# Performance work log

Hardware: AMD Instinct MI355X
Metric: run time of the kernel (lower is better)

Reference implementation:

```python
import jax, jax.numpy as jnp
import numpy as np

D_MODEL = 1024
D_STATE = 32
K = 4
B_SZ = 2
L_SEQ = 1024
DT_MIN = 0.001
DT_MAX = 0.2


def setup_inputs() -> dict:
    key = jax.random.key(0)
    ks = jax.random.split(key, 10)
    n = lambda k, s: jax.random.normal(k, s, dtype=jnp.float32)
    D, N = D_MODEL, D_STATE
    return {
        "x": n(ks[0], (B_SZ, L_SEQ, D)),
        "W_in": 0.02 * n(ks[1], (D, 2 * D)),
        "b_in": jnp.zeros((2 * D,), jnp.float32),
        "conv_w": 0.2 * n(ks[2], (D, 1, K)),   # depthwise conv kernel (O,I/g,K)
        "conv_b": jnp.zeros((D,), jnp.float32),
        "A_log": -2.0 + 0.1 * n(ks[3], (D, N)),
        "wB": 0.02 * n(ks[4], (D, N)),
        "bB": jnp.zeros((D, N), jnp.float32),
        "wC": 0.02 * n(ks[5], (D, N)),
        "bC": jnp.zeros((D, N), jnp.float32),
        "W_dt": 0.02 * n(ks[6], (D, D)),
        "b_dt": jnp.zeros((D,), jnp.float32),
        "W_out": 0.02 * n(ks[7], (D, D)),
        "b_out": jnp.zeros((D,), jnp.float32),
        "ln_g": jnp.ones((D,), jnp.float32),
        "ln_b": jnp.zeros((D,), jnp.float32),
    }


def reference(x, W_in, b_in, conv_w, conv_b, A_log, wB, bB, wC, bC,
              W_dt, b_dt, W_out, b_out, ln_g, ln_b):
    Bsz, L, D = x.shape
    N = A_log.shape[1]
    residual = x
    # input projection -> x path and gate z
    xz = x @ W_in + b_in
    xp, z = jnp.split(xz, 2, axis=-1)
    # causal depthwise conv1d (left-pad k-1)
    xt = jnp.swapaxes(xp, 1, 2)  # (B, D, L)
    y = jax.lax.conv_general_dilated(
        xt, conv_w, window_strides=(1,), padding=[(K - 1, 0)],
        dimension_numbers=("NCH", "OIH", "NCH"), feature_group_count=D)
    x_conv = jnp.swapaxes(y + conv_b[None, :, None], 1, 2)  # (B, L, D)
    xs = jax.nn.silu(x_conv)
    # selective SSM parameters
    A = -jnp.exp(jnp.clip(A_log, -5.0, 2.0))          # (D, N)
    Bt = xs[..., None] * wB + bB                      # (B, L, D, N) grouped 1x1 conv
    Ct = xs[..., None] * wC + bC                      # (B, L, D, N)
    dt = jnp.clip(jax.nn.softplus(xs @ W_dt + b_dt), DT_MIN, DT_MAX)  # (B, L, D)

    def step(states, inp):
        dt_i, B_i, C_i, x_i = inp  # (B,D), (B,D,N), (B,D,N), (B,D)
        A_bar = jnp.exp(jnp.clip(dt_i[..., None] * A, -10.0, 0.0))
        st = jnp.clip(states * A_bar + dt_i[..., None] * B_i * x_i[..., None],
                      -10.0, 10.0)
        return st, jnp.sum(C_i * st, axis=-1)

    states0 = jnp.zeros((Bsz, D, N), x.dtype)
    tl = lambda a: jnp.moveaxis(a, 1, 0)  # time-leading for scan
    _, ys = jax.lax.scan(step, states0, (tl(dt), tl(Bt), tl(Ct), tl(xs)))
    scan_out = jnp.moveaxis(ys, 0, 1) * jax.nn.silu(z)  # (B, L, D)
    out = scan_out @ W_out + b_out
    h = out + residual
    mu = jnp.mean(h, axis=-1, keepdims=True)
    var = jnp.var(h, axis=-1, keepdims=True)
    return (h - mu) / jnp.sqrt(var + 1e-5) * ln_g + ln_b
```

## Files before the change

### kernel.cpp

```cpp
#include <hip/hip_runtime.h>
#include <hip/hip_bf16.h>
#include <math.h>

#define D_MODEL 1024
#define D_STATE 32
#define LSEQ    1024
#define BSZ     2
#define MROWS   (BSZ*LSEQ)
#define NSEG    32
#define SEGL    (LSEQ/NSEG)
#define SCD     8
#define LOG2E   1.4426950408889634f

typedef unsigned short u16;
typedef unsigned int   u32;
typedef __bf16 bf16x8 __attribute__((ext_vector_type(8)));
typedef float  f32x4  __attribute__((ext_vector_type(4)));

__device__ __forceinline__ u16 f2b(float v) {
    unsigned int b = __float_as_uint(v);
    return (u16)((b + 0x7FFFu + ((b >> 16) & 1u)) >> 16);
}
__device__ __forceinline__ float b2f(u16 v) {
    return __uint_as_float((unsigned)v << 16);
}
__device__ __forceinline__ float softplus_clip(float v) {
    float sp = fmaxf(v, 0.f) + log1pf(__expf(-fabsf(v)));
    return fminf(fmaxf(sp, 0.001f), 0.2f);
}
__device__ __forceinline__ float silu(float v) {
    return v / (1.f + __expf(-v));
}

#define GLOAD16(g, l) __builtin_amdgcn_global_load_lds(                     \
    (__attribute__((address_space(1))) void*)(g),                           \
    (__attribute__((address_space(3))) void*)(l), 16, 0, 0)

__global__ __launch_bounds__(256)
void wprep_k(const float* __restrict__ W_in, const float* __restrict__ W_dt,
             const float* __restrict__ W_out, const float* __restrict__ x,
             u16* __restrict__ WinT, u16* __restrict__ WdtT,
             u16* __restrict__ WoutT, u16* __restrict__ xb) {
    int job = blockIdx.x;
    if (job >= 4096) {
        int i = (job - 4096) * 256 + threadIdx.x;
        float4 v = ((const float4*)x)[i];
        ushort4 o;
        o.x = f2b(v.x); o.y = f2b(v.y); o.z = f2b(v.z); o.w = f2b(v.w);
        ((ushort4*)xb)[i] = o;
        return;
    }
    const float* W; u16* Wt; int N;
    if (job < 2048)      { W = W_in;  Wt = WinT;  N = 2048; }
    else if (job < 3072) { W = W_dt;  Wt = WdtT;  N = 1024; job -= 2048; }
    else                 { W = W_out; Wt = WoutT; N = 1024; job -= 3072; }
    const int K = 1024;
    const int ntx = N >> 5;
    const int n0 = (job % ntx) << 5, k0 = (job / ntx) << 5;
    __shared__ u16 tile[32][33];
    const int tx = threadIdx.x & 31, ty = threadIdx.x >> 5;
#pragma unroll
    for (int r = 0; r < 32; r += 8)
        tile[r + ty][tx] = f2b(W[(size_t)(k0 + r + ty) * N + n0 + tx]);
    __syncthreads();
#pragma unroll
    for (int r = 0; r < 32; r += 8)
        Wt[(size_t)(n0 + r + ty) * K + k0 + tx] = tile[tx][r + ty];
}

template<int EPI, int OD>
__global__ __launch_bounds__(256)
void mgemm2_k(const u16* __restrict__ A, const u16* __restrict__ Bt,
              const float* __restrict__ bias, const float* __restrict__ res,
              void* __restrict__ Cv, int M, int N, int K) {
    __shared__ u16 As[2][4096];
    __shared__ u16 Bs[2][4096];
    const int t  = threadIdx.x;
    const int l  = t & 63;
    const int w  = t >> 6;
    const int wr = w >> 1, wc = w & 1;
    const int fr = l & 15, fq = l >> 4;

    const int nx  = N >> 6;
    const int nwg = (M >> 6) * nx;
    int wg = blockIdx.y * nx + blockIdx.x;
    int sw = (wg & 7) * (nwg >> 3) + (wg >> 3);
    const int bm = (sw / nx) << 6;
    const int bn = (sw % nx) << 6;

    const int srow = t >> 3;
    const int scol = ((t & 7) * 8) ^ ((srow & 7) << 3);
    const u16* Ap0 = A  + (size_t)(bm + srow)      * K + scol;
    const u16* Ap1 = A  + (size_t)(bm + 32 + srow) * K + scol;
    const u16* Bp0 = Bt + (size_t)(bn + srow)      * K + scol;
    const u16* Bp1 = Bt + (size_t)(bn + 32 + srow) * K + scol;

    f32x4 acc[2][2] = {};

#define STAGE2(buf, k0)                                      \
    GLOAD16(Ap0 + (k0), &As[buf][t * 8]);                    \
    GLOAD16(Ap1 + (k0), &As[buf][2048 + t * 8]);             \
    GLOAD16(Bp0 + (k0), &Bs[buf][t * 8]);                    \
    GLOAD16(Bp1 + (k0), &Bs[buf][2048 + t * 8]);

    STAGE2(0, 0)
    asm volatile("s_waitcnt vmcnt(0)" ::: "memory");
    __syncthreads();

    const int NT = K >> 6;
    int cur = 0;
    for (int ks = 0; ks < NT; ++ks) {
        if (ks + 1 < NT) { STAGE2(cur ^ 1, (ks + 1) << 6) }
        bf16x8 af[2][2], bf[2][2];
#pragma unroll
        for (int m = 0; m < 2; ++m) {
            const int r = wr * 32 + m * 16 + fr;
            const int xo = (r & 7) << 3;
#pragma unroll
            for (int kk = 0; kk < 2; ++kk)
                af[m][kk] = *(const bf16x8*)&As[cur][r * 64 + ((kk * 32 + fq * 8) ^ xo)];
        }
#pragma unroll
        for (int n = 0; n < 2; ++n) {
            const int c = wc * 32 + n * 16 + fr;
            const int xo = (c & 7) << 3;
#pragma unroll
            for (int kk = 0; kk < 2; ++kk)
                bf[n][kk] = *(const bf16x8*)&Bs[cur][c * 64 + ((kk * 32 + fq * 8) ^ xo)];
        }
#pragma unroll
        for (int m = 0; m < 2; ++m)
#pragma unroll
            for (int n = 0; n < 2; ++n)
#pragma unroll
                for (int kk = 0; kk < 2; ++kk)
                    acc[m][n] = __builtin_amdgcn_mfma_f32_16x16x32_bf16(
                        af[m][kk], bf[n][kk], acc[m][n], 0, 0, 0);
        asm volatile("s_waitcnt vmcnt(0)" ::: "memory");
        __syncthreads();
        cur ^= 1;
    }
#undef STAGE2

#pragma unroll
    for (int m = 0; m < 2; ++m) {
        const int row = bm + wr * 32 + m * 16 + fq * 4;
#pragma unroll
        for (int n = 0; n < 2; ++n) {
            const int col = bn + wc * 32 + n * 16 + fr;
            float bi = (EPI == 3) ? 0.f : bias[col];
#pragma unroll
            for (int j = 0; j < 4; ++j) {
                float v = acc[m][n][j];
                if (EPI == 3) v = softplus_clip(v + bias[row + j]);
                else          v += bi;
                if (EPI == 2) v += res[(size_t)(row + j) * N + col];
                if (OD == 1) ((u16*)Cv)[(size_t)(row + j) * N + col] = f2b(v);
                else         ((float*)Cv)[(size_t)(row + j) * N + col] = v;
            }
        }
    }
}

__global__ __launch_bounds__(256)
void convT_k(const u16* __restrict__ xz, const float* __restrict__ cw,
             const float* __restrict__ cb,
             u16* __restrict__ xsb, u16* __restrict__ xsT,
             u16* __restrict__ zsT) {
    const int l0 = blockIdx.x * 64;
    const int d0 = blockIdx.y * 64;
    const int b  = blockIdx.z;
    const int t  = threadIdx.x;
    __shared__ float xin[67][68];
    __shared__ float xo[64][69];
    const int lr = t >> 4, c4 = (t & 15) << 2;
    const u16* srcx = xz + ((size_t)b * LSEQ + l0 - 3) * 2048 + d0;
#pragma unroll
    for (int p = 0; p < 5; ++p) {
        int r = p * 16 + lr;
        if (r < 67) {
            float4 v = make_float4(0.f, 0.f, 0.f, 0.f);
            if (l0 + r >= 3) {
                ushort4 u = *(const ushort4*)(srcx + (size_t)r * 2048 + c4);
                v = make_float4(b2f(u.x), b2f(u.y), b2f(u.z), b2f(u.w));
            }
            *(float4*)&xin[r][c4] = v;
        }
    }
    __syncthreads();
    const int dd = t & 63;
    const int wv = t >> 6;
    float4 w4 = *(const float4*)(cw + ((size_t)(d0 + dd)) * 4);
    float cbv = cb[d0 + dd];
    float win[19];
#pragma unroll
    for (int i = 0; i < 19; ++i) win[i] = xin[wv * 16 + i][dd];
    u16* xrow = xsb + ((size_t)b * LSEQ + l0 + wv * 16) * D_MODEL + d0 + dd;
#pragma unroll
    for (int i = 0; i < 16; ++i) {
        float a = cbv;
        a = fmaf(win[i],     w4.x, a);
        a = fmaf(win[i + 1], w4.y, a);
        a = fmaf(win[i + 2], w4.z, a);
        a = fmaf(win[i + 3], w4.w, a);
        float r = silu(a);
        xrow[(size_t)i * D_MODEL] = f2b(r);
        xo[dd][wv * 16 + i] = r;
    }
    __syncthreads();
    {
        const int dr = t >> 2, ls = (t & 3) << 4;
        u16* dst = xsT + ((size_t)(d0 + dr)) * MROWS + (size_t)b * LSEQ + l0 + ls;
        ushort4 o[4];
#pragma unroll
        for (int j = 0; j < 16; ++j)
            ((u16*)o)[j] = f2b(xo[dr][ls + j]);
#pragma unroll
        for (int j = 0; j < 4; ++j)
            ((ushort4*)dst)[j] = o[j];
    }
    __syncthreads();
    const u16* srcz = xz + ((size_t)b * LSEQ + l0) * 2048 + 1024 + d0;
#pragma unroll
    for (int p = 0; p < 4; ++p) {
        int r = p * 16 + lr;
        ushort4 u = *(const ushort4*)(srcz + (size_t)r * 2048 + c4);
        xo[c4 + 0][r] = silu(b2f(u.x));
        xo[c4 + 1][r] = silu(b2f(u.y));
        xo[c4 + 2][r] = silu(b2f(u.z));
        xo[c4 + 3][r] = silu(b2f(u.w));
    }
    __syncthreads();
    {
        const int dr = t >> 2, ls = (t & 3) << 4;
        u16* dst = zsT + ((size_t)(d0 + dr)) * MROWS + (size_t)b * LSEQ + l0 + ls;
        ushort4 o[4];
#pragma unroll
        for (int j = 0; j < 16; ++j)
            ((u16*)o)[j] = f2b(xo[dr][ls + j]);
#pragma unroll
        for (int j = 0; j < 4; ++j)
            ((ushort4*)dst)[j] = o[j];
    }
}

__global__ __launch_bounds__(256, 4)
void scan_a(const u16* __restrict__ xsT, const u16* __restrict__ dtT,
            const float* __restrict__ A_log, const float* __restrict__ wB,
            const float* __restrict__ bB,
            float* __restrict__ Qbuf, float* __restrict__ sdtb) {
    const int t   = threadIdx.x;
    const int grp = t >> 5, g = t & 31;
    const int d   = blockIdx.x * SCD + grp;
    const int seg = blockIdx.y, b = blockIdx.z;
    const size_t chb = (size_t)d * MROWS + (size_t)b * LSEQ + (size_t)seg * SEGL;
    const int pi  = d * D_STATE + g;

    const float A2  = -__expf(fminf(fmaxf(A_log[pi], -5.f), 2.f)) * LOG2E;
    const float wB0 = wB[pi], bB0 = bB[pi];
    float s = 0.f;

    u16 xu = xsT[chb + g];
    u16 du = dtT[chb + g];
    float sdt = b2f(du);
    u32 pk = ((u32)xu << 16) | du;
#pragma unroll
    for (int h = 0; h < 2; ++h) {
        float av[16], dbv[16];
#pragma unroll
        for (int u = 0; u < 16; ++u) {
            u32 p = (u32)__shfl((int)pk, h * 16 + u, 32);
            float xa = __uint_as_float(p & 0xffff0000u);
            float da = __uint_as_float(p << 16);
            av[u]  = __builtin_amdgcn_exp2f(da * A2);
            dbv[u] = (da * xa) * fmaf(xa, wB0, bB0);
        }
#pragma unroll
        for (int u = 0; u < 16; ++u)
            s = fmaf(s, av[u], dbv[u]);
    }
    sdt += __shfl_xor(sdt, 1);
    sdt += __shfl_xor(sdt, 2);
    sdt += __shfl_xor(sdt, 4);
    sdt += __shfl_xor(sdt, 8);
    sdt += __shfl_xor(sdt, 16);
    const size_t qb = ((size_t)b * D_MODEL + d) * NSEG + seg;
    Qbuf[qb * 32 + g] = s;
    if (g == 0) sdtb[qb] = sdt;
}

__global__ __launch_bounds__(256, 4)
void scan_c(const u16* __restrict__ xsT, const u16* __restrict__ dtT,
            const u16* __restrict__ zsT,
            const float* __restrict__ A_log, const float* __restrict__ wB,
            const float* __restrict__ bB, const float* __restrict__ wC,
            const float* __restrict__ bC,
            const float* __restrict__ Qbuf, const float* __restrict__ sdtb,
            u16* __restrict__ so) {
    const int t   = threadIdx.x;
    const int grp = t >> 5, g = t & 31;
    const int d   = blockIdx.x * SCD + grp;
    const int seg = blockIdx.y, b = blockIdx.z;
    const size_t chb = (size_t)d * MROWS + (size_t)b * LSEQ + (size_t)seg * SEGL;
    const int pi  = d * D_STATE + g;

    const float A2  = -__expf(fminf(fmaxf(A_log[pi], -5.f), 2.f)) * LOG2E;
    const float wB0 = wB[pi], bB0 = bB[pi];
    const float wC0 = wC[pi], bC0 = bC[pi];

    float s = 0.f;
    const size_t qb = ((size_t)b * D_MODEL + d) * NSEG;
    for (int j = 0; j < seg; ++j) {
        float qj = Qbuf[(qb + j) * 32 + g];
        float pj = __builtin_amdgcn_exp2f(A2 * sdtb[qb + j]);
        s = fmaf(s, pj, qj);
    }

    __shared__ u16 tile[32][10];
    const size_t obase = ((size_t)b * LSEQ + (size_t)seg * SEGL) * D_MODEL
                       + blockIdx.x * SCD;

    {
        u16 xu = xsT[chb + g];
        u16 du = dtT[chb + g];
        float zw = b2f(zsT[chb + g]);
        u32 pk = ((u32)xu << 16) | du;
        float w_[32];
#pragma unroll
        for (int h = 0; h < 2; ++h) {
            float av[16], dbv[16], cv[16];
#pragma unroll
            for (int u = 0; u < 16; ++u) {
                u32 p = (u32)__shfl((int)pk, h * 16 + u, 32);
                float xa = __uint_as_float(p & 0xffff0000u);
                float da = __uint_as_float(p << 16);
                av[u]  = __builtin_amdgcn_exp2f(da * A2);
                dbv[u] = (da * xa) * fmaf(xa, wB0, bB0);
                cv[u]  = fmaf(xa, wC0, bC0);
            }
#pragma unroll
            for (int u = 0; u < 16; ++u) {
                s = fmaf(s, av[u], dbv[u]);
                w_[h * 16 + u] = cv[u] * s;
            }
        }
#pragma unroll
        for (int u = 0; u < 16; ++u) {
            float snd = (g & 16) ? w_[u] : w_[u + 16];
            float rcv = __shfl_xor(snd, 16);
            w_[u] = ((g & 16) ? w_[u + 16] : w_[u]) + rcv;
        }
#pragma unroll
        for (int u = 0; u < 8; ++u) {
            float snd = (g & 8) ? w_[u] : w_[u + 8];
            float rcv = __shfl_xor(snd, 8);
            w_[u] = ((g & 8) ? w_[u + 8] : w_[u]) + rcv;
        }
#pragma unroll
        for (int u = 0; u < 4; ++u) {
            float snd = (g & 4) ? w_[u] : w_[u + 4];
            float rcv = __shfl_xor(snd, 4);
            w_[u] = ((g & 4) ? w_[u + 4] : w_[u]) + rcv;
        }
#pragma unroll
        for (int u = 0; u < 2; ++u) {
            float snd = (g & 2) ? w_[u] : w_[u + 2];
            float rcv = __shfl_xor(snd, 2);
            w_[u] = ((g & 2) ? w_[u + 2] : w_[u]) + rcv;
        }
        {
            float snd = (g & 1) ? w_[0] : w_[1];
            float rcv = __shfl_xor(snd, 1);
            w_[0] = ((g & 1) ? w_[1] : w_[0]) + rcv;
        }
        float sv = w_[0] * zw;
        __syncthreads();
        tile[g][grp] = f2b(sv);
        __syncthreads();
        {
            int i = t >> 3, j = t & 7;
            so[obase + (size_t)i * D_MODEL + j] = tile[i][j];
        }
    }
}

__global__ __launch_bounds__(256)
void ln_k(const float* __restrict__ h, const float* __restrict__ gam,
          const float* __restrict__ bet, float* __restrict__ out) {
    int row = blockIdx.x;
    const float* hr = h + (size_t)row * D_MODEL;
    int t = threadIdx.x;
    float4 v = *(const float4*)(hr + (t << 2));
    float s  = v.x + v.y + v.z + v.w;
    float ss = v.x * v.x + v.y * v.y + v.z * v.z + v.w * v.w;
#pragma unroll
    for (int m = 1; m < 64; m <<= 1) {
        s  += __shfl_xor(s,  m, 64);
        ss += __shfl_xor(ss, m, 64);
    }
    __shared__ float red[8];
    int wid = t >> 6, lane = t & 63;
    if (lane == 0) { red[wid] = s; red[4 + wid] = ss; }
    __syncthreads();
    s  = red[0] + red[1] + red[2] + red[3];
    ss = red[4] + red[5] + red[6] + red[7];
    float mu  = s * (1.f / D_MODEL);
    float var = ss * (1.f / D_MODEL) - mu * mu;
    float r = rsqrtf(var + 1e-5f);
    float4 g4 = *(const float4*)(gam + (t << 2));
    float4 b4 = *(const float4*)(bet + (t << 2));
    float4 o;
    o.x = (v.x - mu) * r * g4.x + b4.x;
    o.y = (v.y - mu) * r * g4.y + b4.y;
    o.z = (v.z - mu) * r * g4.z + b4.z;
    o.w = (v.w - mu) * r * g4.w + b4.w;
    *(float4*)(out + (size_t)row * D_MODEL + (t << 2)) = o;
}

extern "C" void kernel_launch(void* const* d_in, const int* in_sizes, int n_in,
                              void* d_out, int out_size, void* d_ws, size_t ws_size,
                              hipStream_t stream) {
    const float* x      = (const float*)d_in[0];
    const float* W_in   = (const float*)d_in[1];
    const float* b_in   = (const float*)d_in[2];
    const float* conv_w = (const float*)d_in[3];
    const float* conv_b = (const float*)d_in[4];
    const float* A_log  = (const float*)d_in[5];
    const float* wB     = (const float*)d_in[6];
    const float* bB     = (const float*)d_in[7];
    const float* wC     = (const float*)d_in[8];
    const float* bC     = (const float*)d_in[9];
    const float* W_dt   = (const float*)d_in[10];
    const float* b_dt   = (const float*)d_in[11];
    const float* W_out  = (const float*)d_in[12];
    const float* b_out  = (const float*)d_in[13];
    const float* ln_g   = (const float*)d_in[14];
    const float* ln_b   = (const float*)d_in[15];
    float* out = (float*)d_out;

    const size_t MB = 1024 * 1024;
    char* w = (char*)d_ws;
    u16*   xz    = (u16*)  (w);
    u16*   xsT   = (u16*)  (w + 8  * MB);
    u16*   zsT   = (u16*)  (w + 12 * MB);
    u16*   xsb16 = (u16*)  (w + 16 * MB);
    u16*   xb    = (u16*)  (w + 20 * MB);
    u16*   WinT  = (u16*)  (w + 24 * MB);
    u16*   WdtT  = (u16*)  (w + 28 * MB);
    u16*   WoutT = (u16*)  (w + 30 * MB);
    u16*   dtT   = (u16*)  (w + 32 * MB);
    float* Qbuf  = (float*)(w + 36 * MB);
    float* sdtb  = (float*)(w + 44 * MB);
    float* hb    = (float*)(w);
    u16*   sob16 = xb;

    dim3 blk(256);
    wprep_k<<<dim3(6144), blk, 0, stream>>>(W_in, W_dt, W_out, x,
                                            WinT, WdtT, WoutT, xb);

    mgemm2_k<0, 1><<<dim3(2048 / 64, MROWS / 64), blk, 0, stream>>>(
        xb, WinT, b_in, nullptr, xz, MROWS, 2048, D_MODEL);
    convT_k<<<dim3(LSEQ / 64, D_MODEL / 64, BSZ), blk, 0, stream>>>(
        xz, conv_w, conv_b, xsb16, xsT, zsT);
    mgemm2_k<3, 1><<<dim3(MROWS / 64, D_MODEL / 64), blk, 0, stream>>>(
        WdtT, xsb16, b_dt, nullptr, dtT, D_MODEL, MROWS, D_MODEL);
    scan_a<<<dim3(D_MODEL / SCD, NSEG, BSZ), blk, 0, stream>>>(
        xsT, dtT, A_log, wB, bB, Qbuf, sdtb);
    scan_c<<<dim3(D_MODEL / SCD, NSEG, BSZ), blk, 0, stream>>>(
        xsT, dtT, zsT, A_log, wB, bB, wC, bC, Qbuf, sdtb, sob16);
    mgemm2_k<2, 0><<<dim3(D_MODEL / 64, MROWS / 64), blk, 0, stream>>>(
        sob16, WoutT, b_out, x, hb, MROWS, D_MODEL, D_MODEL);
    ln_k<<<dim3(MROWS), blk, 0, stream>>>(hb, ln_g, ln_b, out);
}
```

Baseline: 126.2 us.

## Halve scan segment count and add separate inter-segment prefix kernel

Reduces the number of scan segments from 32 to 16, so each segment now covers 64 timesteps processed in a loop of 32-step chunks. A new scan_b kernel computes the exclusive prefix of segment carry states once per channel and state and writes it back into Qbuf. scan_c then loads its starting state directly instead of redoing a serial carry loop over all previous segments. This removes the quadratic redundant carry work in scan_c, at the cost of an extra kernel launch, less parallelism in scan_a and scan_c, and longer serial chains inside each segment.

```diff
diff --git a/kernel.cpp b/kernel.cpp
--- a/kernel.cpp
+++ b/kernel.cpp
@@ -7,7 +7,7 @@
 #define LSEQ    1024
 #define BSZ     2
 #define MROWS   (BSZ*LSEQ)
-#define NSEG    32
+#define NSEG    16
 #define SEGL    (LSEQ/NSEG)
 #define SCD     8
 #define LOG2E   1.4426950408889634f
@@ -258,26 +258,28 @@
 
     const float A2  = -__expf(fminf(fmaxf(A_log[pi], -5.f), 2.f)) * LOG2E;
     const float wB0 = wB[pi], bB0 = bB[pi];
-    float s = 0.f;
-
-    u16 xu = xsT[chb + g];
-    u16 du = dtT[chb + g];
-    float sdt = b2f(du);
-    u32 pk = ((u32)xu << 16) | du;
-#pragma unroll
-    for (int h = 0; h < 2; ++h) {
-        float av[16], dbv[16];
-#pragma unroll
-        for (int u = 0; u < 16; ++u) {
-            u32 p = (u32)__shfl((int)pk, h * 16 + u, 32);
-            float xa = __uint_as_float(p & 0xffff0000u);
-            float da = __uint_as_float(p << 16);
-            av[u]  = __builtin_amdgcn_exp2f(da * A2);
-            dbv[u] = (da * xa) * fmaf(xa, wB0, bB0);
-        }
-#pragma unroll
-        for (int u = 0; u < 16; ++u)
-            s = fmaf(s, av[u], dbv[u]);
+    float s = 0.f, sdt = 0.f;
+
+    for (int l0 = 0; l0 < SEGL; l0 += 32) {
+        u16 xu = xsT[chb + l0 + g];
+        u16 du = dtT[chb + l0 + g];
+        sdt += b2f(du);
+        u32 pk = ((u32)xu << 16) | du;
+#pragma unroll
+        for (int h = 0; h < 2; ++h) {
+            float av[16], dbv[16];
+#pragma unroll
+            for (int u = 0; u < 16; ++u) {
+                u32 p = (u32)__shfl((int)pk, h * 16 + u, 32);
+                float xa = __uint_as_float(p & 0xffff0000u);
+                float da = __uint_as_float(p << 16);
+                av[u]  = __builtin_amdgcn_exp2f(da * A2);
+                dbv[u] = (da * xa) * fmaf(xa, wB0, bB0);
+            }
+#pragma unroll
+            for (int u = 0; u < 16; ++u)
+                s = fmaf(s, av[u], dbv[u]);
+        }
     }
     sdt += __shfl_xor(sdt, 1);
     sdt += __shfl_xor(sdt, 2);
@@ -289,13 +291,32 @@
     if (g == 0) sdtb[qb] = sdt;
 }
 
+__global__ __launch_bounds__(256)
+void scan_b(const float* __restrict__ A_log, const float* __restrict__ sdtb,
+            float* __restrict__ Qbuf) {
+    const int idx = blockIdx.x * 256 + threadIdx.x;
+    const int g   = idx & 31;
+    const int ch  = idx >> 5;
+    const int d   = ch & (D_MODEL - 1);
+    const float A2 = -__expf(fminf(fmaxf(A_log[d * D_STATE + g], -5.f), 2.f)) * LOG2E;
+    const size_t qb = (size_t)ch * NSEG;
+    float s = 0.f;
+#pragma unroll
+    for (int j = 0; j < NSEG; ++j) {
+        float q = Qbuf[(qb + j) * 32 + g];
+        float p = __builtin_amdgcn_exp2f(A2 * sdtb[qb + j]);
+        Qbuf[(qb + j) * 32 + g] = s;
+        s = fmaf(s, p, q);
+    }
+}
+
 __global__ __launch_bounds__(256, 4)
 void scan_c(const u16* __restrict__ xsT, const u16* __restrict__ dtT,
             const u16* __restrict__ zsT,
             const float* __restrict__ A_log, const float* __restrict__ wB,
             const float* __restrict__ bB, const float* __restrict__ wC,
             const float* __restrict__ bC,
-            const float* __restrict__ Qbuf, const float* __restrict__ sdtb,
+            const float* __restrict__ Qbuf,
             u16* __restrict__ so) {
     const int t   = threadIdx.x;
     const int grp = t >> 5, g = t & 31;
@@ -308,22 +329,16 @@
     const float wB0 = wB[pi], bB0 = bB[pi];
     const float wC0 = wC[pi], bC0 = bC[pi];
 
-    float s = 0.f;
-    const size_t qb = ((size_t)b * D_MODEL + d) * NSEG;
-    for (int j = 0; j < seg; ++j) {
-        float qj = Qbuf[(qb + j) * 32 + g];
-        float pj = __builtin_amdgcn_exp2f(A2 * sdtb[qb + j]);
-        s = fmaf(s, pj, qj);
-    }
+    float s = Qbuf[(((size_t)b * D_MODEL + d) * NSEG + seg) * 32 + g];
 
     __shared__ u16 tile[32][10];
     const size_t obase = ((size_t)b * LSEQ + (size_t)seg * SEGL) * D_MODEL
                        + blockIdx.x * SCD;
 
-    {
-        u16 xu = xsT[chb + g];
-        u16 du = dtT[chb + g];
-        float zw = b2f(zsT[chb + g]);
+    for (int l0 = 0; l0 < SEGL; l0 += 32) {
+        u16 xu = xsT[chb + l0 + g];
+        u16 du = dtT[chb + l0 + g];
+        float zw = b2f(zsT[chb + l0 + g]);
         u32 pk = ((u32)xu << 16) | du;
         float w_[32];
 #pragma unroll
@@ -379,7 +394,7 @@
         __syncthreads();
         {
             int i = t >> 3, j = t & 7;
-            so[obase + (size_t)i * D_MODEL + j] = tile[i][j];
+            so[obase + (size_t)(l0 + i) * D_MODEL + j] = tile[i][j];
         }
     }
 }
@@ -450,7 +465,7 @@
     u16*   WoutT = (u16*)  (w + 30 * MB);
     u16*   dtT   = (u16*)  (w + 32 * MB);
     float* Qbuf  = (float*)(w + 36 * MB);
-    float* sdtb  = (float*)(w + 44 * MB);
+    float* sdtb  = (float*)(w + 40 * MB);
     float* hb    = (float*)(w);
     u16*   sob16 = xb;
 
@@ -466,8 +481,10 @@
         WdtT, xsb16, b_dt, nullptr, dtT, D_MODEL, MROWS, D_MODEL);
     scan_a<<<dim3(D_MODEL / SCD, NSEG, BSZ), blk, 0, stream>>>(
         xsT, dtT, A_log, wB, bB, Qbuf, sdtb);
+    scan_b<<<dim3(BSZ * D_MODEL * D_STATE / 256), blk, 0, stream>>>(
+        A_log, sdtb, Qbuf);
     scan_c<<<dim3(D_MODEL / SCD, NSEG, BSZ), blk, 0, stream>>>(
-        xsT, dtT, zsT, A_log, wB, bB, wC, bC, Qbuf, sdtb, sob16);
+        xsT, dtT, zsT, A_log, wB, bB, wC, bC, Qbuf, sob16);
     mgemm2_k<2, 0><<<dim3(D_MODEL / 64, MROWS / 64), blk, 0, stream>>>(
         sob16, WoutT, b_out, x, hb, MROWS, D_MODEL, D_MODEL);
     ln_k<<<dim3(MROWS), blk, 0, stream>>>(hb, ln_g, ln_b, out);
```

New measurement: 116.3 us. -7.9%, faster.
